# Optimization experiments

Measured on AMD Instinct MI355X. Metric: run time of the kernel, lower is better.

Reference implementation:

```python
import jax, jax.numpy as jnp
import numpy as np

N = 131072   # total nodes
G = 4096     # graphs
E = 524288   # directed bond edges
C = 96       # hidden_channels
L = 8        # num_layers
F_IN = 64    # atom features
NT = 5       # targets


def setup_inputs() -> dict:
    key = jax.random.key(0)
    ks = jax.random.split(key, 32)
    def rn(k, shape, s=0.05):
        return jax.random.normal(k, shape, jnp.float32) * s
    inp = {
        'x': jax.random.normal(ks[0], (N, F_IN), jnp.float32),
        'edge_index': jax.random.randint(ks[1], (2, E), 0, N),
        'batch': jnp.sort(jax.random.randint(ks[2], (N,), 0, G)),
        'num_graphs': G,
        # atom encoder
        'enc_w': rn(ks[3], (F_IN, C)), 'enc_b': rn(ks[4], (C,)),
        # virtual node embedding + MLP (Linear->BN->SiLU->Linear)
        'vn_emb': rn(ks[5], (C,)),
        'vn_w1': rn(ks[6], (C, C)), 'vn_b1': rn(ks[7], (C,)),
        'vn_g1': 1.0 + rn(ks[8], (C,)), 'vn_be1': rn(ks[9], (C,)),
        'vn_w2': rn(ks[10], (C, C)), 'vn_b2': rn(ks[11], (C,)),
        # per-layer GIN MLP (Linear C->2C, BN, SiLU, Linear 2C->C) stacked over L
        'conv_w1': rn(ks[12], (L, C, 2 * C)), 'conv_b1': rn(ks[13], (L, 2 * C)),
        'conv_g1': 1.0 + rn(ks[14], (L, 2 * C)), 'conv_be1': rn(ks[15], (L, 2 * C)),
        'conv_w2': rn(ks[16], (L, 2 * C, C)), 'conv_b2': rn(ks[17], (L, C)),
        # per-layer outer BatchNorm
        'bn_g': 1.0 + rn(ks[18], (L, C)), 'bn_b': rn(ks[19], (L, C)),
        # head: C->C/2 (BN,SiLU) -> C/4 (BN,SiLU) -> NT
        'h_w1': rn(ks[20], (C, C // 2)), 'h_b1': rn(ks[21], (C // 2,)),
        'h_g1': 1.0 + rn(ks[22], (C // 2,)), 'h_be1': rn(ks[23], (C // 2,)),
        'h_w2': rn(ks[24], (C // 2, C // 4)), 'h_b2': rn(ks[25], (C // 4,)),
        'h_g2': 1.0 + rn(ks[26], (C // 4,)), 'h_be2': rn(ks[27], (C // 4,)),
        'h_w3': rn(ks[28], (C // 4, NT)), 'h_b3': rn(ks[29], (NT,)),
    }
    return inp


def _bn(x, g, b, eps=1e-5):
    # training-mode BatchNorm1d: biased batch variance (matches torch normalization)
    m = x.mean(0)
    v = x.var(0)
    return (x - m) * jax.lax.rsqrt(v + eps) * g + b


def reference(x, edge_index, batch, num_graphs, enc_w, enc_b, vn_emb,
              vn_w1, vn_b1, vn_g1, vn_be1, vn_w2, vn_b2,
              conv_w1, conv_b1, conv_g1, conv_be1, conv_w2, conv_b2,
              bn_g, bn_b,
              h_w1, h_b1, h_g1, h_be1, h_w2, h_b2, h_g2, h_be2, h_w3, h_b3):
    n = x.shape[0]
    gN = int(num_graphs)
    c = enc_w.shape[1]
    nl = conv_w1.shape[0]

    h = x @ enc_w + enc_b                                   # [n, C]
    vn = jnp.broadcast_to(vn_emb, (gN, c))                  # virtual node feats
    h = jnp.concatenate([h, vn], 0)                         # [n+gN, C]

    # vectorized virtual-node edges: (n+batch[i]) <-> i, both directions
    node_ids = jnp.arange(n, dtype=batch.dtype)
    vidx = n + batch
    src = jnp.concatenate([edge_index[0], vidx, node_ids])
    tgt = jnp.concatenate([edge_index[1], node_ids, vidx])
    total = n + gN

    for i in range(nl):
        # GINConv, eps=0: MLP(x + sum_neighbors)
        agg = jax.ops.segment_sum(h[src], tgt, num_segments=total)
        z = h + agg
        z = z @ conv_w1[i] + conv_b1[i]
        z = jax.nn.silu(_bn(z, conv_g1[i], conv_be1[i]))
        z = z @ conv_w2[i] + conv_b2[i]
        z = jax.nn.silu(_bn(z, bn_g[i], bn_b[i]))           # outer BN + SiLU (dropout=eval)
        h = z if i == 0 else h + z                          # residual after layer 0
        if i < nl - 1:
            v = h[n:]
            v = jax.nn.silu(_bn(v @ vn_w1 + vn_b1, vn_g1, vn_be1)) @ vn_w2 + vn_b2
            h = jnp.concatenate([h[:n], v], 0)

    hn = h[:n]
    sums = jax.ops.segment_sum(hn, batch, num_segments=gN)
    counts = jax.ops.segment_sum(jnp.ones((n,), hn.dtype), batch, num_segments=gN)
    pooled = sums / jnp.maximum(counts, 1.0)[:, None]       # global_mean_pool

    z = jax.nn.silu(_bn(pooled @ h_w1 + h_b1, h_g1, h_be1))
    z = jax.nn.silu(_bn(z @ h_w2 + h_b2, h_g2, h_be2))
    return z @ h_w3 + h_b3                                  # [G, 5]
```

## Files before the change

### kernel.cpp

```cpp
#include <hip/hip_runtime.h>
#include <hip/hip_bf16.h>

constexpr int N_   = 131072;
constexpr int G_   = 4096;
constexpr int E_   = 524288;
constexpr int C_   = 96;
constexpr int L_   = 8;
constexpr int FIN_ = 64;
constexpr int TOT_ = N_ + G_;

typedef __attribute__((ext_vector_type(8))) short short8v;
typedef __attribute__((ext_vector_type(4))) float f32x4;
using bf16 = __hip_bfloat16;

__device__ __forceinline__ float silu_f(float y) { return y / (1.f + __expf(-y)); }
__device__ __forceinline__ float toF(float x) { return x; }
__device__ __forceinline__ float toF(bf16 x)  { return __bfloat162float(x); }
__device__ __forceinline__ float bfbits2f(short s) {
  return __uint_as_float(((unsigned)(unsigned short)s) << 16);
}
__device__ __forceinline__ short f2bfbits(float f) {
  bf16 b = __float2bfloat16(f);
  return *reinterpret_cast<short*>(&b);
}
__device__ __forceinline__ void atomAddD(double* p, double v) { unsafeAtomicAdd(p, v); }
__device__ __forceinline__ void atomAddF(float* p, float v)  { unsafeAtomicAdd(p, v); }

static inline int gblk(long n) { return (int)((n + 255) / 256); }

__global__ __launch_bounds__(256) void k_prep(const float* __restrict__ enc_w,
    const float* __restrict__ conv_w1, const float* __restrict__ conv_w2,
    const float* __restrict__ vn_w1, const float* __restrict__ vn_w2,
    bf16* __restrict__ encwT, bf16* __restrict__ w1T, bf16* __restrict__ w2T,
    bf16* __restrict__ vnw1T, bf16* __restrict__ vnw2T) {
  int idx = blockIdx.x * 256 + threadIdx.x;
  const float* src; bf16* dst; int Kd, Nd, local;
  if (idx < 6144)        { src = enc_w;   dst = encwT; Kd = 64;  Nd = 96;  local = idx; }
  else if (idx < 153600) { src = conv_w1; dst = w1T;   Kd = 96;  Nd = 192; local = idx - 6144; }
  else if (idx < 301056) { src = conv_w2; dst = w2T;   Kd = 192; Nd = 96;  local = idx - 153600; }
  else if (idx < 310272) { src = vn_w1;   dst = vnw1T; Kd = 96;  Nd = 96;  local = idx - 301056; }
  else if (idx < 319488) { src = vn_w2;   dst = vnw2T; Kd = 96;  Nd = 96;  local = idx - 310272; }
  else return;
  int per = Kd * Nd;
  int i   = local / per;
  int rem = local - i * per;
  int k   = rem / Nd;
  int n   = rem - k * Nd;
  dst[(size_t)i * per + n * Kd + k] = __float2bfloat16(src[local]);
}

__global__ __launch_bounds__(256) void k_deg_count(const int* __restrict__ tgt, int* __restrict__ deg) {
  int e = blockIdx.x * 256 + threadIdx.x;
  if (e >= E_) return;
  atomicAdd(&deg[tgt[e]], 1);
}

__global__ __launch_bounds__(256) void k_scan_local(const int* __restrict__ deg, int* __restrict__ lp,
                                                    int* __restrict__ bsum) {
  __shared__ int s[256];
  int t = threadIdx.x;
  int i = blockIdx.x * 256 + t;
  int v = deg[i];
  s[t] = v;
  __syncthreads();
  for (int off = 1; off < 256; off <<= 1) {
    int x = (t >= off) ? s[t - off] : 0;
    __syncthreads();
    s[t] += x;
    __syncthreads();
  }
  lp[i] = s[t] - v;
  if (t == 255) bsum[blockIdx.x] = s[255];
}

__global__ __launch_bounds__(512) void k_scan_bsum(const int* __restrict__ bsum, int* __restrict__ boff) {
  __shared__ int s[512];
  int t = threadIdx.x;
  int v = bsum[t];
  s[t] = v;
  __syncthreads();
  for (int off = 1; off < 512; off <<= 1) {
    int x = (t >= off) ? s[t - off] : 0;
    __syncthreads();
    s[t] += x;
    __syncthreads();
  }
  boff[t] = s[t] - v;
}

__global__ __launch_bounds__(256) void k_scan_add(int* __restrict__ rs, const int* __restrict__ boff) {
  int i = blockIdx.x * 256 + threadIdx.x;
  if (i > N_) return;
  if (i == N_) { rs[N_] = E_; return; }
  rs[i] += boff[i >> 8];
}

__global__ __launch_bounds__(256) void k_csr_fill(const int* __restrict__ src, const int* __restrict__ tgt,
                                                  const int* __restrict__ rs, int* __restrict__ cur,
                                                  int* __restrict__ ssrc) {
  int e = blockIdx.x * 256 + threadIdx.x;
  if (e >= E_) return;
  int t = tgt[e];
  int pos = atomicAdd(&cur[t], 1);
  ssrc[rs[t] + pos] = src[e];
}

__global__ __launch_bounds__(256) void k_gbounds(const int* __restrict__ batch, int* __restrict__ gstart) {
  int i = blockIdx.x * 256 + threadIdx.x;
  if (i > N_) return;
  if (i == N_) {
    int last = batch[N_ - 1];
    for (int g = last + 1; g <= G_; ++g) gstart[g] = N_;
    return;
  }
  int b  = batch[i];
  int bp = (i == 0) ? -1 : batch[i - 1];
  for (int g = bp + 1; g <= b; ++g) gstart[g] = i;
}

__global__ __launch_bounds__(256) void k_deghist(const int* __restrict__ deg, int* __restrict__ hist) {
  __shared__ int lh[33];
  if (threadIdx.x < 33) lh[threadIdx.x] = 0;
  __syncthreads();
  int i = blockIdx.x * 256 + threadIdx.x;
  if (i < N_) {
    int b = deg[i]; if (b > 32) b = 32;
    atomicAdd(&lh[b], 1);
  }
  __syncthreads();
  if (threadIdx.x < 33 && lh[threadIdx.x] != 0) atomicAdd(&hist[threadIdx.x], lh[threadIdx.x]);
}

__global__ __launch_bounds__(64) void k_degbase(const int* __restrict__ hist, int* __restrict__ base) {
  if (threadIdx.x == 0) {
    int acc = 0;
    for (int b = 32; b >= 0; --b) { base[b] = acc; acc += hist[b]; }
  }
}

__global__ __launch_bounds__(256) void k_permfill(const int* __restrict__ deg, const int* __restrict__ base,
                                                  int* __restrict__ curs, int* __restrict__ perm) {
  __shared__ int lh[33];
  __shared__ int lbase[33];
  if (threadIdx.x < 33) lh[threadIdx.x] = 0;
  __syncthreads();
  int i = blockIdx.x * 256 + threadIdx.x;
  int b = 0, lpos = 0;
  bool act = (i < N_);
  if (act) {
    b = deg[i]; if (b > 32) b = 32;
    lpos = atomicAdd(&lh[b], 1);
  }
  __syncthreads();
  if (threadIdx.x < 33) {
    int cnt = lh[threadIdx.x];
    lbase[threadIdx.x] = cnt ? atomicAdd(&curs[threadIdx.x], cnt) : 0;
  }
  __syncthreads();
  if (act) perm[base[b] + lbase[b] + lpos] = i;
}

__global__ __launch_bounds__(192) void k_vnagg(const bf16* __restrict__ hb, const int* __restrict__ gstart,
                                               float* __restrict__ vna) {
  int slot = threadIdx.x / 24;
  int c4   = (threadIdx.x % 24) * 4;
  int g = blockIdx.x * 8 + slot;
  int i0 = gstart[g], i1 = gstart[g + 1];
  float s0 = 0.f, s1 = 0.f, s2 = 0.f, s3 = 0.f;
  for (int i = i0; i < i1; ++i) {
    short4 v = *(const short4*)((const short*)hb + (size_t)i * C_ + c4);
    s0 += bfbits2f(v.x); s1 += bfbits2f(v.y); s2 += bfbits2f(v.z); s3 += bfbits2f(v.w);
  }
  float4 o; o.x = s0; o.y = s1; o.z = s2; o.w = s3;
  *(float4*)(vna + (size_t)g * C_ + c4) = o;
}

template <int K, int NOUT, bool INACT, bool OSTATS, bool AF32, typename OutT>
__global__ __launch_bounds__(512) void k_gemm(const void* __restrict__ Aptr, const bf16* __restrict__ Wt,
                                              const float* __restrict__ bias,
                                              const double* __restrict__ stin,
                                              const float* __restrict__ gam, const float* __restrict__ bet,
                                              float Rin,
                                              OutT* __restrict__ out, double* __restrict__ stout) {
  constexpr int KK  = K / 32;
  constexpr int NT  = NOUT / 16;
  constexpr int UPR = K / 8;
  constexpr int LPR = UPR + 1;
  constexpr int LWB  = NOUT * LPR * 16;
  constexpr int ISCB = INACT ? 2 * K * 4 : 0;
  constexpr int SMB  = LWB + (ISCB > 0 ? ISCB : 1);
  __shared__ __align__(16) char smem[SMB];
  uint4* lw   = reinterpret_cast<uint4*>(smem);
  float* lsc  = reinterpret_cast<float*>(smem + LWB);
  float* lsh  = lsc + K;
  float* ssum = reinterpret_cast<float*>(smem);
  float* sqs  = ssum + 8 * NOUT;

  const uint4* wv = (const uint4*)Wt;
  for (int u = threadIdx.x; u < NOUT * UPR; u += 512) {
    int row = u / UPR, colu = u - row * UPR;
    lw[row * LPR + colu] = wv[u];
  }
  if (INACT) {
    for (int k = threadIdx.x; k < K; k += 512) {
      double mean = stin[k] / (double)Rin;
      double var  = stin[K + k] / (double)Rin - mean * mean;
      float sc = gam[k] * rsqrtf((float)var + 1e-5f);
      lsc[k] = sc;
      lsh[k] = bet[k] - (float)mean * sc;
    }
  }

  int wave = threadIdx.x >> 6, lane = threadIdx.x & 63;
  int m0 = (blockIdx.x * 8 + wave) * 16;
  int lr = lane & 15, lg = lane >> 4;

  short8v a[KK];
  if constexpr (AF32) {
    const float* Arow = (const float*)Aptr + (size_t)(m0 + lr) * K + lg * 8;
#pragma unroll
    for (int kk = 0; kk < KK; ++kk) {
      float4 f0 = *(const float4*)(Arow + kk * 32);
      float4 f1 = *(const float4*)(Arow + kk * 32 + 4);
      a[kk][0] = f2bfbits(f0.x); a[kk][1] = f2bfbits(f0.y);
      a[kk][2] = f2bfbits(f0.z); a[kk][3] = f2bfbits(f0.w);
      a[kk][4] = f2bfbits(f1.x); a[kk][5] = f2bfbits(f1.y);
      a[kk][6] = f2bfbits(f1.z); a[kk][7] = f2bfbits(f1.w);
    }
  } else {
    const short* Arow = (const short*)Aptr + (size_t)(m0 + lr) * K + lg * 8;
#pragma unroll
    for (int kk = 0; kk < KK; ++kk) a[kk] = *(const short8v*)(Arow + kk * 32);
  }

  __syncthreads();

  if (INACT) {
#pragma unroll
    for (int kk = 0; kk < KK; ++kk) {
      int kbase = kk * 32 + lg * 8;
#pragma unroll
      for (int j = 0; j < 8; ++j) {
        float f = bfbits2f(a[kk][j]);
        f = silu_f(fmaf(f, lsc[kbase + j], lsh[kbase + j]));
        a[kk][j] = f2bfbits(f);
      }
    }
  }

  f32x4 acc[NT];
#pragma unroll
  for (int nt = 0; nt < NT; ++nt) acc[nt] = (f32x4){0.f, 0.f, 0.f, 0.f};

#pragma unroll
  for (int nt = 0; nt < NT; ++nt) {
    const short* brow = (const short*)&lw[(nt * 16 + lr) * LPR] + lg * 8;
#pragma unroll
    for (int kk = 0; kk < KK; ++kk) {
      short8v b = *(const short8v*)(brow + kk * 32);
      acc[nt] = __builtin_amdgcn_mfma_f32_16x16x32_bf16(a[kk], b, acc[nt], 0, 0, 0);
    }
  }

  if (OSTATS) __syncthreads();

  int orow = m0 + (lg << 2);
#pragma unroll
  for (int nt = 0; nt < NT; ++nt) {
    int col = nt * 16 + lr;
    float bi = bias[col];
    float s = 0.f, q = 0.f;
#pragma unroll
    for (int r = 0; r < 4; ++r) {
      float y = acc[nt][r] + bi;
      float yb;
      size_t off = (size_t)(orow + r) * NOUT + col;
      if constexpr (sizeof(OutT) == 2) {
        short bits = f2bfbits(y);
        ((short*)out)[off] = bits;
        yb = bfbits2f(bits);
      } else {
        ((float*)out)[off] = y;
        yb = y;
      }
      if (OSTATS) { s += yb; q += yb * yb; }
    }
    if (OSTATS) {
      s += __shfl_xor(s, 16, 64); s += __shfl_xor(s, 32, 64);
      q += __shfl_xor(q, 16, 64); q += __shfl_xor(q, 32, 64);
      if (lg == 0) { ssum[wave * NOUT + col] = s; sqs[wave * NOUT + col] = q; }
    }
  }
  if (OSTATS) {
    __syncthreads();
    int tid = threadIdx.x;
    if (tid < NOUT) {
      float s = 0.f, q = 0.f;
#pragma unroll
      for (int w = 0; w < 8; ++w) { s += ssum[w * NOUT + tid]; q += sqs[w * NOUT + tid]; }
      atomAddD(&stout[tid], (double)s);
      atomAddD(&stout[NOUT + tid], (double)q);
    }
  }
}

template <int K, int NOUT>
__global__ __launch_bounds__(512) void k_gemm_agg(const bf16* __restrict__ hb,
    const int* __restrict__ batch, const int* __restrict__ rs, const int* __restrict__ ssrc,
    const float* __restrict__ vna, const int* __restrict__ perm,
    const bf16* __restrict__ Wt, const float* __restrict__ bias,
    bf16* __restrict__ out, double* __restrict__ st) {
  constexpr int KK  = K / 32;
  constexpr int NT  = NOUT / 16;
  constexpr int UPR = K / 8;
  constexpr int LPR = UPR + 1;
  constexpr int LWB = NOUT * LPR * 16;
  __shared__ __align__(16) char smem[LWB];
  uint4* lw   = reinterpret_cast<uint4*>(smem);
  float* ssum = reinterpret_cast<float*>(smem);
  float* sqs  = ssum + 8 * NOUT;

  const uint4* wv = (const uint4*)Wt;
  for (int u = threadIdx.x; u < NOUT * UPR; u += 512) {
    int row = u / UPR, colu = u - row * UPR;
    lw[row * LPR + colu] = wv[u];
  }

  int wave = threadIdx.x >> 6, lane = threadIdx.x & 63;
  int m0 = (blockIdx.x * 8 + wave) * 16;
  int lr = lane & 15, lg = lane >> 4;
  int row = m0 + lr;
  int rowo = (m0 < N_) ? perm[row] : row;
  int koff = lg * 8;

  float av[KK * 8];
#pragma unroll
  for (int t = 0; t < KK * 8; ++t) av[t] = 0.f;

  auto addPtr = [&](const short* p) {
#pragma unroll
    for (int kk = 0; kk < KK; ++kk) {
      short8v v = *(const short8v*)(p + koff + kk * 32);
#pragma unroll
      for (int j = 0; j < 8; ++j) av[kk * 8 + j] += bfbits2f(v[j]);
    }
  };
  auto addPtr2 = [&](const short* p0, const short* p1) {
    short8v v0[KK], v1[KK];
#pragma unroll
    for (int kk = 0; kk < KK; ++kk) {
      v0[kk] = *(const short8v*)(p0 + koff + kk * 32);
      v1[kk] = *(const short8v*)(p1 + koff + kk * 32);
    }
#pragma unroll
    for (int kk = 0; kk < KK; ++kk)
#pragma unroll
      for (int j = 0; j < 8; ++j)
        av[kk * 8 + j] += bfbits2f(v0[kk][j]) + bfbits2f(v1[kk][j]);
  };
  auto hrow = [&](int r) { return (const short*)hb + (size_t)r * K; };

  if (m0 < N_) {
    addPtr2(hrow(rowo), hrow(N_ + batch[rowo]));
    int e = rs[rowo], e1 = rs[rowo + 1];
    for (; e + 2 <= e1; e += 2) addPtr2(hrow(ssrc[e]), hrow(ssrc[e + 1]));
    if (e < e1) addPtr(hrow(ssrc[e]));
  } else {
    addPtr(hrow(rowo));
    const float* vp = vna + (size_t)(rowo - N_) * K + koff;
#pragma unroll
    for (int kk = 0; kk < KK; ++kk) {
      float4 f0 = *(const float4*)(vp + kk * 32);
      float4 f1 = *(const float4*)(vp + kk * 32 + 4);
      av[kk * 8 + 0] += f0.x; av[kk * 8 + 1] += f0.y; av[kk * 8 + 2] += f0.z; av[kk * 8 + 3] += f0.w;
      av[kk * 8 + 4] += f1.x; av[kk * 8 + 5] += f1.y; av[kk * 8 + 6] += f1.z; av[kk * 8 + 7] += f1.w;
    }
  }

  short8v a[KK];
#pragma unroll
  for (int kk = 0; kk < KK; ++kk)
#pragma unroll
    for (int j = 0; j < 8; ++j) a[kk][j] = f2bfbits(av[kk * 8 + j]);

  __syncthreads();

  f32x4 acc[NT];
#pragma unroll
  for (int nt = 0; nt < NT; ++nt) acc[nt] = (f32x4){0.f, 0.f, 0.f, 0.f};

#pragma unroll
  for (int nt = 0; nt < NT; ++nt) {
    const short* brow = (const short*)&lw[(nt * 16 + lr) * LPR] + lg * 8;
#pragma unroll
    for (int kk = 0; kk < KK; ++kk) {
      short8v b = *(const short8v*)(brow + kk * 32);
      acc[nt] = __builtin_amdgcn_mfma_f32_16x16x32_bf16(a[kk], b, acc[nt], 0, 0, 0);
    }
  }

  __syncthreads();

  int rid[4];
#pragma unroll
  for (int r = 0; r < 4; ++r) rid[r] = __shfl(rowo, (lg << 2) + r, 64);

#pragma unroll
  for (int nt = 0; nt < NT; ++nt) {
    int col = nt * 16 + lr;
    float bi = bias[col];
    float s = 0.f, q = 0.f;
#pragma unroll
    for (int r = 0; r < 4; ++r) {
      float y = acc[nt][r] + bi;
      short bits = f2bfbits(y);
      ((short*)out)[(size_t)rid[r] * NOUT + col] = bits;
      float yb = bfbits2f(bits);
      s += yb; q += yb * yb;
    }
    s += __shfl_xor(s, 16, 64); s += __shfl_xor(s, 32, 64);
    q += __shfl_xor(q, 16, 64); q += __shfl_xor(q, 32, 64);
    if (lg == 0) { ssum[wave * NOUT + col] = s; sqs[wave * NOUT + col] = q; }
  }
  __syncthreads();
  int tid = threadIdx.x;
  if (tid < NOUT) {
    float s = 0.f, q = 0.f;
#pragma unroll
    for (int w = 0; w < 8; ++w) { s += ssum[w * NOUT + tid]; q += sqs[w * NOUT + tid]; }
    atomAddD(&st[tid], (double)s);
    atomAddD(&st[NOUT + tid], (double)q);
  }
}

__global__ __launch_bounds__(256) void k_fill_vn(bf16* __restrict__ hb, const float* __restrict__ vn) {
  int idx = blockIdx.x * 256 + threadIdx.x;
  if (idx >= G_ * C_) return;
  int c = idx % C_;
  hb[(size_t)N_ * C_ + idx] = __float2bfloat16(vn[c]);
}

template <int CC, typename T>
__global__ __launch_bounds__(256) void k_bnstats(const T* __restrict__ X, int R, double* __restrict__ st) {
  int c = threadIdx.x;
  float s = 0.f, q = 0.f;
  for (int r = blockIdx.x; r < R; r += gridDim.x) {
    float v = toF(X[(size_t)r * CC + c]);
    s += v;
    q += v * v;
  }
  atomAddD(&st[c], (double)s);
  atomAddD(&st[CC + c], (double)q);
}

template <int CC>
__global__ __launch_bounds__(256) void k_bnfin(const double* __restrict__ st, int R,
    const float* __restrict__ g, const float* __restrict__ be,
    float* __restrict__ scale, float* __restrict__ shift) {
  int c = threadIdx.x;
  if (c >= CC) return;
  double mean = st[c] / R;
  double var  = st[CC + c] / R - mean * mean;
  float sc = g[c] * rsqrtf((float)var + 1e-5f);
  scale[c] = sc;
  shift[c] = be[c] - (float)mean * sc;
}

__global__ __launch_bounds__(192) void k_update(const bf16* __restrict__ Z, bf16* __restrict__ hb,
    const double* __restrict__ st,
    const float* __restrict__ gam, const float* __restrict__ bet, int addResid,
    float* __restrict__ vna, const int* __restrict__ batch, int accvna) {
  __shared__ float lsc[C_], lsh[C_];
  __shared__ float lh[16][C_];
  __shared__ int   lbatch[16];
  int t = threadIdx.x;
  if (t < C_) {
    double mean = st[t] / (double)TOT_;
    double var  = st[C_ + t] / (double)TOT_ - mean * mean;
    float sc = gam[t] * rsqrtf((float)var + 1e-5f);
    lsc[t] = sc;
    lsh[t] = bet[t] - (float)mean * sc;
  }
  int r0 = blockIdx.x * 16;
  int nodeBlk = (r0 < N_);
  if (accvna && nodeBlk && t < 16) lbatch[t] = batch[r0 + t];
  __syncthreads();

  int rl = t / 12;
  int cg = t - rl * 12;
  int c0 = cg * 8;
  size_t vidx = (size_t)(r0 + rl) * 12 + cg;
  short8v zv = ((const short8v*)Z)[vidx];
  short8v hv = ((const short8v*)hb)[vidx];
  short8v o;
  float hn[8];
#pragma unroll
  for (int j = 0; j < 8; ++j) {
    float y = silu_f(fmaf(bfbits2f(zv[j]), lsc[c0 + j], lsh[c0 + j]));
    hn[j] = addResid ? (bfbits2f(hv[j]) + y) : y;
    o[j] = f2bfbits(hn[j]);
  }
  ((short8v*)hb)[vidx] = o;

  if (accvna && nodeBlk) {
#pragma unroll
    for (int j = 0; j < 8; ++j) lh[rl][c0 + j] = hn[j];
    __syncthreads();
    if (t < C_) {
      int c = t;
      float run = 0.f;
      int g = lbatch[0];
      for (int r = 0; r < 16; ++r) {
        int gb = lbatch[r];
        if (gb != g) { atomAddF(&vna[(size_t)g * C_ + c], run); run = 0.f; g = gb; }
        run += lh[r][c];
      }
      atomAddF(&vna[(size_t)g * C_ + c], run);
    }
  }
}

template <int K, int M, bool INACT>
__global__ __launch_bounds__(256) void k_mm(const float* __restrict__ A,
    const float* __restrict__ W, const float* __restrict__ bias,
    const float* __restrict__ isc, const float* __restrict__ ish,
    float* __restrict__ out, int R) {
  int idx = blockIdx.x * 256 + threadIdx.x;
  if (idx >= R * M) return;
  int row = idx / M;
  int m   = idx - row * M;
  const float* ar = A + (size_t)row * K;
  float s = bias[m];
#pragma unroll 8
  for (int k = 0; k < K; ++k) {
    float a = ar[k];
    if (INACT) a = silu_f(fmaf(a, isc[k], ish[k]));
    s = fmaf(a, W[k * M + m], s);
  }
  out[idx] = s;
}

__global__ __launch_bounds__(256) void k_pool2(const bf16* __restrict__ hb, const int* __restrict__ gstart,
                                               float* __restrict__ pooled) {
  int idx = blockIdx.x * 256 + threadIdx.x;
  if (idx >= G_ * C_) return;
  int g = idx / C_;
  int c = idx - g * C_;
  int i0 = gstart[g], i1 = gstart[g + 1];
  float s = 0.f;
  for (int i = i0; i < i1; ++i) s += toF(hb[(size_t)i * C_ + c]);
  pooled[idx] = s / fmaxf((float)(i1 - i0), 1.0f);
}

extern "C" void kernel_launch(void* const* d_in, const int* in_sizes, int n_in,
                              void* d_out, int out_size, void* d_ws, size_t ws_size,
                              hipStream_t stream) {
  (void)in_sizes; (void)n_in; (void)out_size; (void)ws_size;
  const float* x       = (const float*)d_in[0];
  const int*   ei      = (const int*)d_in[1];
  const int*   batch   = (const int*)d_in[2];
  const float* enc_w   = (const float*)d_in[4];
  const float* enc_b   = (const float*)d_in[5];
  const float* vn_emb  = (const float*)d_in[6];
  const float* vn_w1   = (const float*)d_in[7];
  const float* vn_b1   = (const float*)d_in[8];
  const float* vn_g1   = (const float*)d_in[9];
  const float* vn_be1  = (const float*)d_in[10];
  const float* vn_w2   = (const float*)d_in[11];
  const float* vn_b2   = (const float*)d_in[12];
  const float* conv_w1 = (const float*)d_in[13];
  const float* conv_b1 = (const float*)d_in[14];
  const float* conv_g1 = (const float*)d_in[15];
  const float* conv_be1= (const float*)d_in[16];
  const float* conv_w2 = (const float*)d_in[17];
  const float* conv_b2 = (const float*)d_in[18];
  const float* bn_g    = (const float*)d_in[19];
  const float* bn_b    = (const float*)d_in[20];
  const float* h_w1    = (const float*)d_in[21];
  const float* h_b1    = (const float*)d_in[22];
  const float* h_g1    = (const float*)d_in[23];
  const float* h_be1   = (const float*)d_in[24];
  const float* h_w2    = (const float*)d_in[25];
  const float* h_b2    = (const float*)d_in[26];
  const float* h_g2    = (const float*)d_in[27];
  const float* h_be2   = (const float*)d_in[28];
  const float* h_w3    = (const float*)d_in[29];
  const float* h_b3    = (const float*)d_in[30];
  float* out = (float*)d_out;

  const int* e_src = ei;
  const int* e_tgt = ei + E_;

  char* p = (char*)d_ws;
  auto alloc = [&](size_t bytes) -> char* {
    char* r = p;
    p += (bytes + 15) & ~size_t(15);
    return r;
  };
  bf16*   hbf    = (bf16*)  alloc((size_t)TOT_ * C_ * 2);
  float*  vnaf   = (float*) alloc((size_t)G_ * C_ * 4);
  bf16*   vtb    = (bf16*)  alloc((size_t)G_ * C_ * 2);
  float*  pooled = (float*) alloc((size_t)G_ * C_ * 4);
  float*  t1     = (float*) alloc((size_t)G_ * 48 * 4);
  float*  t2     = (float*) alloc((size_t)G_ * 24 * 4);
  float*  scale1 = (float*) alloc(256 * 4);
  float*  shift1 = (float*) alloc(256 * 4);
  float*  scale2 = (float*) alloc(256 * 4);
  float*  shift2 = (float*) alloc(256 * 4);
  double* stbuf  = (double*)alloc((size_t)26 * 384 * 8);
  bf16*   z1     = (bf16*)  alloc((size_t)TOT_ * 2 * C_ * 2);
  bf16*   z2     = (bf16*)  alloc((size_t)TOT_ * C_ * 2);
  bf16*   encwT  = (bf16*)  alloc((size_t)C_ * FIN_ * 2);
  bf16*   w1T    = (bf16*)  alloc((size_t)L_ * 2 * C_ * C_ * 2);
  bf16*   w2T    = (bf16*)  alloc((size_t)L_ * C_ * 2 * C_ * 2);
  bf16*   vnw1T  = (bf16*)  alloc((size_t)C_ * C_ * 2);
  bf16*   vnw2T  = (bf16*)  alloc((size_t)C_ * C_ * 2);
  int*    deg    = (int*)   alloc((size_t)N_ * 4);
  int*    cur    = (int*)   alloc((size_t)N_ * 4);
  int*    rs     = (int*)   alloc((size_t)(N_ + 1) * 4);
  int*    bsum   = (int*)   alloc(512 * 4);
  int*    boff   = (int*)   alloc(512 * 4);
  int*    ssrc   = (int*)   alloc((size_t)E_ * 4);
  int*    gstart = (int*)   alloc((size_t)(G_ + 1) * 4);
  int*    perm   = (int*)   alloc((size_t)N_ * 4);
  int*    hist   = (int*)   alloc(33 * 4);
  int*    hbase  = (int*)   alloc(33 * 4);
  int*    hcurs  = (int*)   alloc(33 * 4);

  auto ST = [&](int i) { return stbuf + (size_t)i * 384; };

  k_prep<<<gblk(319488), 256, 0, stream>>>(enc_w, conv_w1, conv_w2, vn_w1, vn_w2,
                                           encwT, w1T, w2T, vnw1T, vnw2T);

  hipMemsetAsync(deg, 0, (size_t)N_ * 4, stream);
  hipMemsetAsync(cur, 0, (size_t)N_ * 4, stream);
  hipMemsetAsync(stbuf, 0, (size_t)26 * 384 * 8, stream);
  hipMemsetAsync(hist, 0, 33 * 4, stream);
  hipMemsetAsync(hcurs, 0, 33 * 4, stream);
  k_deg_count<<<gblk(E_), 256, 0, stream>>>(e_tgt, deg);
  k_scan_local<<<N_ / 256, 256, 0, stream>>>(deg, rs, bsum);
  k_scan_bsum<<<1, 512, 0, stream>>>(bsum, boff);
  k_scan_add<<<gblk(N_ + 1), 256, 0, stream>>>(rs, boff);
  k_csr_fill<<<gblk(E_), 256, 0, stream>>>(e_src, e_tgt, rs, cur, ssrc);
  k_gbounds<<<gblk(N_ + 1), 256, 0, stream>>>(batch, gstart);
  k_deghist<<<gblk(N_), 256, 0, stream>>>(deg, hist);
  k_degbase<<<1, 64, 0, stream>>>(hist, hbase);
  k_permfill<<<gblk(N_), 256, 0, stream>>>(deg, hbase, hcurs, perm);

  k_gemm<FIN_, C_, false, false, true, bf16><<<N_ / 128, 512, 0, stream>>>(
      x, encwT, enc_b, nullptr, nullptr, nullptr, 1.f, hbf, nullptr);
  k_fill_vn<<<gblk((long)G_ * C_), 256, 0, stream>>>(hbf, vn_emb);
  k_vnagg<<<G_ / 8, 192, 0, stream>>>(hbf, gstart, vnaf);

  for (int i = 0; i < L_; ++i) {
    const bf16*  wt1 = w1T + (size_t)i * 2 * C_ * C_;
    const bf16*  wt2 = w2T + (size_t)i * C_ * 2 * C_;
    const float* b1  = conv_b1 + (size_t)i * 2 * C_;
    const float* g1  = conv_g1 + (size_t)i * 2 * C_;
    const float* be1 = conv_be1+ (size_t)i * 2 * C_;
    const float* b2  = conv_b2 + (size_t)i * C_;
    const float* bg  = bn_g    + (size_t)i * C_;
    const float* bb  = bn_b    + (size_t)i * C_;
    int accvna = (i < L_ - 1);

    k_gemm_agg<C_, 2 * C_><<<TOT_ / 128, 512, 0, stream>>>(
        hbf, batch, rs, ssrc, vnaf, perm, wt1, b1, z1, ST(i));

    k_gemm<2 * C_, C_, true, true, false, bf16><<<TOT_ / 128, 512, 0, stream>>>(
        z1, wt2, b2, ST(i), g1, be1, (float)TOT_, z2, ST(8 + i));

    if (accvna) hipMemsetAsync(vnaf, 0, (size_t)G_ * C_ * 4, stream);
    k_update<<<TOT_ / 16, 192, 0, stream>>>(z2, hbf, ST(8 + i), bg, bb, i > 0,
                                            vnaf, batch, accvna);

    if (i < L_ - 1) {
      k_gemm<C_, C_, false, true, false, bf16><<<G_ / 128, 512, 0, stream>>>(
          hbf + (size_t)N_ * C_, vnw1T, vn_b1, nullptr, nullptr, nullptr, 1.f, vtb, ST(16 + i));
      k_gemm<C_, C_, true, false, false, bf16><<<G_ / 128, 512, 0, stream>>>(
          vtb, vnw2T, vn_b2, ST(16 + i), vn_g1, vn_be1, (float)G_,
          hbf + (size_t)N_ * C_, nullptr);
    }
  }

  k_pool2<<<gblk((long)G_ * C_), 256, 0, stream>>>(hbf, gstart, pooled);

  k_mm<C_, 48, false><<<gblk((long)G_ * 48), 256, 0, stream>>>(
      pooled, h_w1, h_b1, nullptr, nullptr, t1, G_);
  k_bnstats<48, float><<<64, 48, 0, stream>>>(t1, G_, ST(23));
  k_bnfin<48><<<1, 48, 0, stream>>>(ST(23), G_, h_g1, h_be1, scale1, shift1);

  k_mm<48, 24, true><<<gblk((long)G_ * 24), 256, 0, stream>>>(
      t1, h_w2, h_b2, scale1, shift1, t2, G_);
  k_bnstats<24, float><<<64, 24, 0, stream>>>(t2, G_, ST(24));
  k_bnfin<24><<<1, 24, 0, stream>>>(ST(24), G_, h_g2, h_be2, scale2, shift2);

  k_mm<24, 5, true><<<gblk((long)G_ * 5), 256, 0, stream>>>(
      t2, h_w3, h_b3, scale2, shift2, out, G_);
}
```

Before: 1.162 ms.

## Make aggregation GEMM persistent with atomic work-stealing over row tiles

The fused aggregate+GEMM kernel now launches a fixed grid of 768 blocks, and each wave repeatedly claims a 16-row tile through a global atomic counter (one counter per layer) until all tiles are done. The weight tile is staged into LDS once per block instead of once per 128 rows, and the per-wave BN statistics accumulate in dedicated LDS before a single atomic flush per block. This targets load imbalance from variable node degrees and the repeated weight loads and stat atomics, at the cost of one extra atomic per tile and larger shared memory use.

```diff
diff --git a/kernel.cpp b/kernel.cpp
--- a/kernel.cpp
+++ b/kernel.cpp
@@ -309,125 +309,137 @@
     const int* __restrict__ batch, const int* __restrict__ rs, const int* __restrict__ ssrc,
     const float* __restrict__ vna, const int* __restrict__ perm,
     const bf16* __restrict__ Wt, const float* __restrict__ bias,
-    bf16* __restrict__ out, double* __restrict__ st) {
+    bf16* __restrict__ out, double* __restrict__ st, int* __restrict__ ctr) {
   constexpr int KK  = K / 32;
   constexpr int NT  = NOUT / 16;
   constexpr int UPR = K / 8;
   constexpr int LPR = UPR + 1;
   constexpr int LWB = NOUT * LPR * 16;
-  __shared__ __align__(16) char smem[LWB];
-  uint4* lw   = reinterpret_cast<uint4*>(smem);
-  float* ssum = reinterpret_cast<float*>(smem);
-  float* sqs  = ssum + 8 * NOUT;
+  constexpr int STW = 8 * NOUT;
+  __shared__ __align__(16) char smem[LWB + 2 * STW * 4];
+  uint4* lw    = reinterpret_cast<uint4*>(smem);
+  float* lds_s = reinterpret_cast<float*>(smem + LWB);
+  float* lds_q = lds_s + STW;
 
   const uint4* wv = (const uint4*)Wt;
   for (int u = threadIdx.x; u < NOUT * UPR; u += 512) {
     int row = u / UPR, colu = u - row * UPR;
     lw[row * LPR + colu] = wv[u];
   }
+  for (int u = threadIdx.x; u < STW; u += 512) { lds_s[u] = 0.f; lds_q[u] = 0.f; }
+  __syncthreads();
 
   int wave = threadIdx.x >> 6, lane = threadIdx.x & 63;
-  int m0 = (blockIdx.x * 8 + wave) * 16;
   int lr = lane & 15, lg = lane >> 4;
-  int row = m0 + lr;
-  int rowo = (m0 < N_) ? perm[row] : row;
   int koff = lg * 8;
 
-  float av[KK * 8];
-#pragma unroll
-  for (int t = 0; t < KK * 8; ++t) av[t] = 0.f;
-
-  auto addPtr = [&](const short* p) {
-#pragma unroll
-    for (int kk = 0; kk < KK; ++kk) {
-      short8v v = *(const short8v*)(p + koff + kk * 32);
-#pragma unroll
-      for (int j = 0; j < 8; ++j) av[kk * 8 + j] += bfbits2f(v[j]);
-    }
-  };
-  auto addPtr2 = [&](const short* p0, const short* p1) {
-    short8v v0[KK], v1[KK];
-#pragma unroll
-    for (int kk = 0; kk < KK; ++kk) {
-      v0[kk] = *(const short8v*)(p0 + koff + kk * 32);
-      v1[kk] = *(const short8v*)(p1 + koff + kk * 32);
-    }
+  auto hrow = [&](int r) { return (const short*)hb + (size_t)r * K; };
+
+  for (;;) {
+    int it;
+    if (lane == 0) it = atomicAdd(ctr, 1);
+    it = __shfl(it, 0, 64);
+    if (it >= TOT_ / 16) break;
+
+    int m0 = it * 16;
+    int row = m0 + lr;
+    int rowo = (m0 < N_) ? perm[row] : row;
+
+    float av[KK * 8];
+#pragma unroll
+    for (int t = 0; t < KK * 8; ++t) av[t] = 0.f;
+
+    auto addPtr = [&](const short* p) {
+#pragma unroll
+      for (int kk = 0; kk < KK; ++kk) {
+        short8v v = *(const short8v*)(p + koff + kk * 32);
+#pragma unroll
+        for (int j = 0; j < 8; ++j) av[kk * 8 + j] += bfbits2f(v[j]);
+      }
+    };
+    auto addPtr2 = [&](const short* p0, const short* p1) {
+      short8v v0[KK], v1[KK];
+#pragma unroll
+      for (int kk = 0; kk < KK; ++kk) {
+        v0[kk] = *(const short8v*)(p0 + koff + kk * 32);
+        v1[kk] = *(const short8v*)(p1 + koff + kk * 32);
+      }
+#pragma unroll
+      for (int kk = 0; kk < KK; ++kk)
+#pragma unroll
+        for (int j = 0; j < 8; ++j)
+          av[kk * 8 + j] += bfbits2f(v0[kk][j]) + bfbits2f(v1[kk][j]);
+    };
+
+    if (m0 < N_) {
+      addPtr2(hrow(rowo), hrow(N_ + batch[rowo]));
+      int e = rs[rowo], e1 = rs[rowo + 1];
+      for (; e + 2 <= e1; e += 2) addPtr2(hrow(ssrc[e]), hrow(ssrc[e + 1]));
+      if (e < e1) addPtr(hrow(ssrc[e]));
+    } else {
+      addPtr(hrow(rowo));
+      const float* vp = vna + (size_t)(rowo - N_) * K + koff;
+#pragma unroll
+      for (int kk = 0; kk < KK; ++kk) {
+        float4 f0 = *(const float4*)(vp + kk * 32);
+        float4 f1 = *(const float4*)(vp + kk * 32 + 4);
+        av[kk * 8 + 0] += f0.x; av[kk * 8 + 1] += f0.y; av[kk * 8 + 2] += f0.z; av[kk * 8 + 3] += f0.w;
+        av[kk * 8 + 4] += f1.x; av[kk * 8 + 5] += f1.y; av[kk * 8 + 6] += f1.z; av[kk * 8 + 7] += f1.w;
+      }
+    }
+
+    short8v a[KK];
 #pragma unroll
     for (int kk = 0; kk < KK; ++kk)
 #pragma unroll
-      for (int j = 0; j < 8; ++j)
-        av[kk * 8 + j] += bfbits2f(v0[kk][j]) + bfbits2f(v1[kk][j]);
-  };
-  auto hrow = [&](int r) { return (const short*)hb + (size_t)r * K; };
-
-  if (m0 < N_) {
-    addPtr2(hrow(rowo), hrow(N_ + batch[rowo]));
-    int e = rs[rowo], e1 = rs[rowo + 1];
-    for (; e + 2 <= e1; e += 2) addPtr2(hrow(ssrc[e]), hrow(ssrc[e + 1]));
-    if (e < e1) addPtr(hrow(ssrc[e]));
-  } else {
-    addPtr(hrow(rowo));
-    const float* vp = vna + (size_t)(rowo - N_) * K + koff;
-#pragma unroll
-    for (int kk = 0; kk < KK; ++kk) {
-      float4 f0 = *(const float4*)(vp + kk * 32);
-      float4 f1 = *(const float4*)(vp + kk * 32 + 4);
-      av[kk * 8 + 0] += f0.x; av[kk * 8 + 1] += f0.y; av[kk * 8 + 2] += f0.z; av[kk * 8 + 3] += f0.w;
-      av[kk * 8 + 4] += f1.x; av[kk * 8 + 5] += f1.y; av[kk * 8 + 6] += f1.z; av[kk * 8 + 7] += f1.w;
-    }
-  }
-
-  short8v a[KK];
-#pragma unroll
-  for (int kk = 0; kk < KK; ++kk)
-#pragma unroll
-    for (int j = 0; j < 8; ++j) a[kk][j] = f2bfbits(av[kk * 8 + j]);
-
-  __syncthreads();
-
-  f32x4 acc[NT];
-#pragma unroll
-  for (int nt = 0; nt < NT; ++nt) acc[nt] = (f32x4){0.f, 0.f, 0.f, 0.f};
-
-#pragma unroll
-  for (int nt = 0; nt < NT; ++nt) {
-    const short* brow = (const short*)&lw[(nt * 16 + lr) * LPR] + lg * 8;
-#pragma unroll
-    for (int kk = 0; kk < KK; ++kk) {
-      short8v b = *(const short8v*)(brow + kk * 32);
-      acc[nt] = __builtin_amdgcn_mfma_f32_16x16x32_bf16(a[kk], b, acc[nt], 0, 0, 0);
-    }
-  }
-
-  __syncthreads();
-
-  int rid[4];
-#pragma unroll
-  for (int r = 0; r < 4; ++r) rid[r] = __shfl(rowo, (lg << 2) + r, 64);
-
-#pragma unroll
-  for (int nt = 0; nt < NT; ++nt) {
-    int col = nt * 16 + lr;
-    float bi = bias[col];
-    float s = 0.f, q = 0.f;
-#pragma unroll
-    for (int r = 0; r < 4; ++r) {
-      float y = acc[nt][r] + bi;
-      short bits = f2bfbits(y);
-      ((short*)out)[(size_t)rid[r] * NOUT + col] = bits;
-      float yb = bfbits2f(bits);
-      s += yb; q += yb * yb;
-    }
-    s += __shfl_xor(s, 16, 64); s += __shfl_xor(s, 32, 64);
-    q += __shfl_xor(q, 16, 64); q += __shfl_xor(q, 32, 64);
-    if (lg == 0) { ssum[wave * NOUT + col] = s; sqs[wave * NOUT + col] = q; }
-  }
+      for (int j = 0; j < 8; ++j) a[kk][j] = f2bfbits(av[kk * 8 + j]);
+
+    f32x4 acc[NT];
+#pragma unroll
+    for (int nt = 0; nt < NT; ++nt) acc[nt] = (f32x4){0.f, 0.f, 0.f, 0.f};
+
+#pragma unroll
+    for (int nt = 0; nt < NT; ++nt) {
+      const short* brow = (const short*)&lw[(nt * 16 + lr) * LPR] + lg * 8;
+#pragma unroll
+      for (int kk = 0; kk < KK; ++kk) {
+        short8v b = *(const short8v*)(brow + kk * 32);
+        acc[nt] = __builtin_amdgcn_mfma_f32_16x16x32_bf16(a[kk], b, acc[nt], 0, 0, 0);
+      }
+    }
+
+    int rid[4];
+#pragma unroll
+    for (int r = 0; r < 4; ++r) rid[r] = __shfl(rowo, (lg << 2) + r, 64);
+
+#pragma unroll
+    for (int nt = 0; nt < NT; ++nt) {
+      int col = nt * 16 + lr;
+      float bi = bias[col];
+      float s = 0.f, q = 0.f;
+#pragma unroll
+      for (int r = 0; r < 4; ++r) {
+        float y = acc[nt][r] + bi;
+        short bits = f2bfbits(y);
+        ((short*)out)[(size_t)rid[r] * NOUT + col] = bits;
+        float yb = bfbits2f(bits);
+        s += yb; q += yb * yb;
+      }
+      s += __shfl_xor(s, 16, 64); s += __shfl_xor(s, 32, 64);
+      q += __shfl_xor(q, 16, 64); q += __shfl_xor(q, 32, 64);
+      if (lg == 0) {
+        lds_s[wave * NOUT + col] += s;
+        lds_q[wave * NOUT + col] += q;
+      }
+    }
+  }
+
   __syncthreads();
   int tid = threadIdx.x;
   if (tid < NOUT) {
     float s = 0.f, q = 0.f;
 #pragma unroll
-    for (int w = 0; w < 8; ++w) { s += ssum[w * NOUT + tid]; q += sqs[w * NOUT + tid]; }
+    for (int w = 0; w < 8; ++w) { s += lds_s[w * NOUT + tid]; q += lds_q[w * NOUT + tid]; }
     atomAddD(&st[tid], (double)s);
     atomAddD(&st[NOUT + tid], (double)q);
   }
@@ -626,6 +638,7 @@
   int*    hist   = (int*)   alloc(33 * 4);
   int*    hbase  = (int*)   alloc(33 * 4);
   int*    hcurs  = (int*)   alloc(33 * 4);
+  int*    aggctr = (int*)   alloc(32 * 4);
 
   auto ST = [&](int i) { return stbuf + (size_t)i * 384; };
 
@@ -637,6 +650,7 @@
   hipMemsetAsync(stbuf, 0, (size_t)26 * 384 * 8, stream);
   hipMemsetAsync(hist, 0, 33 * 4, stream);
   hipMemsetAsync(hcurs, 0, 33 * 4, stream);
+  hipMemsetAsync(aggctr, 0, 32 * 4, stream);
   k_deg_count<<<gblk(E_), 256, 0, stream>>>(e_tgt, deg);
   k_scan_local<<<N_ / 256, 256, 0, stream>>>(deg, rs, bsum);
   k_scan_bsum<<<1, 512, 0, stream>>>(bsum, boff);
@@ -663,8 +677,8 @@
     const float* bb  = bn_b    + (size_t)i * C_;
     int accvna = (i < L_ - 1);
 
-    k_gemm_agg<C_, 2 * C_><<<TOT_ / 128, 512, 0, stream>>>(
-        hbf, batch, rs, ssrc, vnaf, perm, wt1, b1, z1, ST(i));
+    k_gemm_agg<C_, 2 * C_><<<768, 512, 0, stream>>>(
+        hbf, batch, rs, ssrc, vnaf, perm, wt1, b1, z1, ST(i), aggctr + i);
 
     k_gemm<2 * C_, C_, true, true, false, bf16><<<TOT_ / 128, 512, 0, stream>>>(
         z1, wt2, b2, ST(i), g1, be1, (float)TOT_, z2, ST(8 + i));
```

After: 2.187 ms, median of 2. 1.88x slower.
